# Kernel optimization log

Hardware: AMD Instinct MI355X
Metric: run time of the kernel (lower is better)

The kernel has to match this reference:

```python
import jax, jax.numpy as jnp
import numpy as np

EPS = 1e-5

def _graph_conv(x, src, dst, W, b, N):
    # DGL GraphConv, norm='both': D_out^{-1/2} then aggregate then D_in^{-1/2}
    ones = jnp.ones((src.shape[0],), x.dtype)
    out_deg = jnp.clip(jax.ops.segment_sum(ones, src, num_segments=N), 1.0)
    in_deg = jnp.clip(jax.ops.segment_sum(ones, dst, num_segments=N), 1.0)
    h = (x * (out_deg ** -0.5)[:, None]) @ W          # [N, out] (mult W before gather)
    agg = jax.ops.segment_sum(h[src], dst, num_segments=N)  # [N, out] irregular scatter
    return agg * (in_deg ** -0.5)[:, None] + b

def _bn_relu(h, gamma, beta):
    # BatchNorm1d in training mode: batch stats over node axis (biased var)
    mu = jnp.mean(h, axis=0)
    var = jnp.mean((h - mu) ** 2, axis=0)
    return jax.nn.relu((h - mu) * jax.lax.rsqrt(var + EPS) * gamma + beta)

def setup_inputs() -> dict:
    key = jax.random.key(0)
    ks = jax.random.split(key, 6)
    N, E, F, H, C = 100000, 1000000, 128, 128, 16
    return {
        "x": jax.random.normal(ks[0], (N, F), dtype=jnp.float32),
        "src": jax.random.randint(ks[1], (E,), 0, N, dtype=jnp.int32),
        "dst": jax.random.randint(ks[2], (E,), 0, N, dtype=jnp.int32),
        "W1": jax.random.normal(ks[3], (F, H), dtype=jnp.float32) * 0.05,
        "b1": jnp.zeros((H,), jnp.float32),
        "g1": jnp.ones((H,), jnp.float32),
        "be1": jnp.zeros((H,), jnp.float32),
        "W2": jax.random.normal(ks[4], (H, H), dtype=jnp.float32) * 0.05,
        "b2": jnp.zeros((H,), jnp.float32),
        "g2": jnp.ones((H,), jnp.float32),
        "be2": jnp.zeros((H,), jnp.float32),
        "Wc": jax.random.normal(ks[5], (H, C), dtype=jnp.float32) * 0.05,
        "bc": jnp.zeros((C,), jnp.float32),
    }

def reference(x, src, dst, W1, b1, g1, be1, W2, b2, g2, be2, Wc, bc):
    N = x.shape[0]
    h = _bn_relu(_graph_conv(x, src, dst, W1, b1, N), g1, be1)  # dropout = identity (eval)
    h = _bn_relu(_graph_conv(h, src, dst, W2, b2, N), g2, be2)
    return h @ Wc + bc  # [N, num_cls]
```

## Files before the change

kernel.cpp:

```cpp
#include <hip/hip_runtime.h>

#define FDIM 128
#define MAXDEG 64
#define GATHERB 2048
#define NREP 32

#define RSIZE 128
#define RSHIFT 7
#define RCAP 1024
#define CCAP 14336
#define PCAP 80
#define WCONVB 8

typedef unsigned short ushort_t;
typedef unsigned int uint_t;
typedef __attribute__((ext_vector_type(8))) short short8;
typedef __attribute__((ext_vector_type(16))) float float16;

__device__ __forceinline__ float bflo(uint_t u) { return __uint_as_float(u << 16); }
__device__ __forceinline__ float bfhi(uint_t u) { return __uint_as_float(u & 0xffff0000u); }
__device__ __forceinline__ ushort_t f2bf(float f) {
    uint_t u = __float_as_uint(f);
    return (ushort_t)((u + 0x7fffu + ((u >> 16) & 1u)) >> 16);
}
__device__ __forceinline__ uint_t pack2bf(float lo, float hi) {
    return (uint_t)f2bf(lo) | ((uint_t)f2bf(hi) << 16);
}

__global__ __launch_bounds__(256) void gemm1_kernel(
    const float* __restrict__ x, const ushort_t* __restrict__ wb,
    const int* __restrict__ cs,
    ushort_t* __restrict__ outb, int N) {
    __shared__ ushort_t zt[64][136];
    __shared__ ushort_t wt[128][136];
    __shared__ float csh[64];
    int t = threadIdx.x;
    int base = blockIdx.x * 64;

    const uint4* wb4 = (const uint4*)wb;
    for (int i = t; i < FDIM * 16; i += 256) {
        int n = i >> 4, q = i & 15;
        *(uint4*)&wt[n][q * 8] = wb4[n * 16 + q];
    }
    if (t < 64) {
        int g = base + t;
        csh[t] = (g < N) ? rsqrtf((float)max(cs[g], 1)) : 1.f;
    }
    const float4* x4 = (const float4*)x;
    for (int i = t; i < 64 * 32; i += 256) {
        int row = i >> 5, c4 = i & 31;
        int grow = base + row;
        uint2 o = make_uint2(0u, 0u);
        if (grow < N) {
            float4 v = x4[(size_t)grow * 32 + c4];
            o.x = pack2bf(v.x, v.y);
            o.y = pack2bf(v.z, v.w);
        }
        *(uint2*)&zt[row][c4 * 4] = o;
    }
    __syncthreads();

    int wv = t >> 6, lane = t & 63;
    int rt = wv >> 1;
    int m = lane & 31;
    int kg = lane >> 5;

    short8 af[8];
#pragma unroll
    for (int kk = 0; kk < 8; kk++)
        af[kk] = *(const short8*)&zt[rt * 32 + m][kk * 16 + kg * 8];

#pragma unroll
    for (int cc = 0; cc < 2; cc++) {
        int ct = (wv & 1) * 2 + cc;
        float16 acc = {0, 0, 0, 0, 0, 0, 0, 0, 0, 0, 0, 0, 0, 0, 0, 0};
#pragma unroll
        for (int kk = 0; kk < 8; kk++) {
            short8 bf = *(const short8*)&wt[ct * 32 + m][kk * 16 + kg * 8];
            acc = __builtin_amdgcn_mfma_f32_32x32x16_bf16(af[kk], bf, acc, 0, 0, 0);
        }
        int col = ct * 32 + m;
#pragma unroll
        for (int r = 0; r < 16; r++) {
            int rl = rt * 32 + (r & 3) + 8 * (r >> 2) + 4 * kg;
            int row = base + rl;
            if (row < N) outb[(size_t)row * FDIM + col] = f2bf(acc[r] * csh[rl]);
        }
    }
}

__global__ __launch_bounds__(256) void bucket_kernel(
    const int* __restrict__ src, const int* __restrict__ dst,
    uint_t* __restrict__ bktD, int* __restrict__ baseD,
    uint_t* __restrict__ bktS, int* __restrict__ baseS,
    const float* __restrict__ W1, const float* __restrict__ W2,
    ushort_t* __restrict__ wb1, ushort_t* __restrict__ wb2,
    int E, int P, int R) {
    __shared__ uint4 buf4[CCAP / 4];
    __shared__ int hist[RCAP];
    __shared__ int scanbuf[256];
    uint_t* buf = (uint_t*)buf4;
    int t = threadIdx.x;

    if (blockIdx.x >= 2 * P) {
        int t0 = (blockIdx.x - 2 * P) * 256 + t;
        for (int i = t0; i < FDIM * FDIM; i += WCONVB * 256) {
            int k = i >> 7, n = i & 127;
            wb1[n * FDIM + k] = f2bf(W1[i]);
            wb2[n * FDIM + k] = f2bf(W2[i]);
        }
        return;
    }

    int role = blockIdx.x >= P;
    int p = role ? blockIdx.x - P : blockIdx.x;
    const int* key = role ? src : dst;
    int e0 = p * CCAP;
    int e1 = min(E, e0 + CCAP);
    int cnt = e1 - e0;

    for (int r = t; r < R; r += 256) hist[r] = 0;
    __syncthreads();
    for (int i = e0 + t; i < e1; i += 256) atomicAdd(&hist[key[i] >> RSHIFT], 1);
    __syncthreads();

    int b0 = t * 4;
    int hv[4];
    int s0 = 0;
#pragma unroll
    for (int k = 0; k < 4; k++) {
        hv[k] = (b0 + k < R) ? hist[b0 + k] : 0;
        s0 += hv[k];
    }
    scanbuf[t] = s0;
    __syncthreads();
    for (int off = 1; off < 256; off <<= 1) {
        int v = (t >= off) ? scanbuf[t - off] : 0;
        __syncthreads();
        scanbuf[t] += v;
        __syncthreads();
    }
    int run = scanbuf[t] - s0;
    int* baseG = role ? baseS : baseD;
#pragma unroll
    for (int k = 0; k < 4; k++) {
        if (b0 + k < R) {
            baseG[(b0 + k) * P + p] = run;
            hist[b0 + k] = run;
        }
        run += hv[k];
    }
    if (t == 0) baseG[R * P + p] = cnt;
    __syncthreads();

    for (int i = e0 + t; i < e1; i += 256) {
        int kv = key[i];
        int slot = atomicAdd(&hist[kv >> RSHIFT], 1);
        uint_t entry = role ? (uint_t)kv
                            : (((uint_t)(kv & (RSIZE - 1)) << 25) | (uint_t)src[i]);
        buf[slot] = entry;
    }
    __syncthreads();

    uint_t* outp = role ? bktS : bktD;
    uint4* og = (uint4*)(outp + (size_t)e0);
    int n4 = (cnt + 3) >> 2;
    for (int j = t; j < n4; j += 256) og[j] = buf4[j];
}

__global__ __launch_bounds__(256) void build_kernel(
    const uint_t* __restrict__ bktD, const int* __restrict__ baseD,
    const uint_t* __restrict__ bktS, const int* __restrict__ baseS,
    int* __restrict__ eidx, int* __restrict__ cnt, int* __restrict__ cs,
    int N, int P) {
    __shared__ uint4 ell4[RSIZE][MAXDEG / 4];
    __shared__ int cntN[RSIZE], csN[RSIZE];
    __shared__ int dB0[PCAP], dB1[PCAP], sB0[PCAP], sB1[PCAP];
    uint_t* ell = (uint_t*)ell4;
    int t = threadIdx.x;
    int r = blockIdx.x;

    if (t < RSIZE) { cntN[t] = 0; csN[t] = 0; }
    for (int i = t; i < P; i += 256) {
        dB0[i] = baseD[r * P + i];
        dB1[i] = baseD[(r + 1) * P + i];
        sB0[i] = baseS[r * P + i];
        sB1[i] = baseS[(r + 1) * P + i];
    }
    __syncthreads();

    int wave = t >> 6, lane = t & 63;
    for (int p = wave; p < P; p += 4) {
        int b = dB0[p], len = dB1[p] - b;
        const uint_t* seg = bktD + (size_t)p * CCAP + b;
        for (int i = lane; i < len; i += 64) {
            uint_t e = seg[i];
            int dl = e >> 25;
            uint_t s = e & 0x1FFFFFFu;
            int slot = atomicAdd(&cntN[dl], 1);
            if (slot < MAXDEG) ell[dl * MAXDEG + slot] = s;
        }
        int b2 = sB0[p], len2 = sB1[p] - b2;
        const uint_t* seg2 = bktS + (size_t)p * CCAP + b2;
        for (int i = lane; i < len2; i += 64)
            atomicAdd(&csN[seg2[i] & (RSIZE - 1)], 1);
    }
    __syncthreads();

    int base = r * RSIZE;
    for (int i = t; i < RSIZE * (MAXDEG / 4); i += 256) {
        int n = i >> 4, q = i & 15;
        int g = base + n;
        if (g < N && q * 4 < min(cntN[n], MAXDEG))
            ((uint4*)eidx)[(size_t)g * (MAXDEG / 4) + q] = ell4[n][q];
    }
    if (t < RSIZE) {
        int g = base + t;
        if (g < N) { cnt[g] = cntN[t]; cs[g] = csN[t]; }
    }
}

__global__ __launch_bounds__(256) void gather_kernel(const ushort_t* __restrict__ hb,
                                                     const int* __restrict__ eidx,
                                                     const int* __restrict__ cnt,
                                                     const float* __restrict__ b,
                                                     ushort_t* __restrict__ outb,
                                                     float* __restrict__ statsRep, int N) {
    __shared__ float4 redS[256];
    __shared__ float4 redQ[256];
    int t = threadIdx.x;
    int wave = t >> 6, lane = t & 63;
    int half = lane >> 5, sub = lane & 31;
    const int STRIDE = GATHERB * 4;
    int gw = blockIdx.x * 4 + wave;
    const uint2* h2 = (const uint2*)hb;
    uint2* o2 = (uint2*)outb;
    float4 bb = ((const float4*)b)[sub];
    float st0 = 0, st1 = 0, st2 = 0, st3 = 0, sq0 = 0, sq1 = 0, sq2 = 0, sq3 = 0;

    int node = gw;
    int deg = 0, ridx = 0;
    if (node < N) {
        deg = cnt[node];
        ridx = eidx[(size_t)node * MAXDEG + lane];
    }
    while (node < N) {
        int nnode = node + STRIDE;
        int ndeg = 0, nridx = 0;
        if (nnode < N) {
            ndeg = cnt[nnode];
            nridx = eidx[(size_t)nnode * MAXDEG + lane];
        }

        int e = min(deg, MAXDEG);
        float a0 = 0, a1 = 0, a2 = 0, a3 = 0;
        float c0 = 0, c1 = 0, c2 = 0, c3 = 0;
        int j = 0;
        for (; j + 7 < e; j += 8) {
            int iA = __shfl(ridx, j + half);
            int iB = __shfl(ridx, j + 2 + half);
            int iC = __shfl(ridx, j + 4 + half);
            int iD = __shfl(ridx, j + 6 + half);
            uint2 uA = h2[(size_t)iA * 32 + sub];
            uint2 uB = h2[(size_t)iB * 32 + sub];
            uint2 uC = h2[(size_t)iC * 32 + sub];
            uint2 uD = h2[(size_t)iD * 32 + sub];
            a0 += bflo(uA.x); a1 += bfhi(uA.x); a2 += bflo(uA.y); a3 += bfhi(uA.y);
            c0 += bflo(uB.x); c1 += bfhi(uB.x); c2 += bflo(uB.y); c3 += bfhi(uB.y);
            a0 += bflo(uC.x); a1 += bfhi(uC.x); a2 += bflo(uC.y); a3 += bfhi(uC.y);
            c0 += bflo(uD.x); c1 += bfhi(uD.x); c2 += bflo(uD.y); c3 += bfhi(uD.y);
        }
        for (; j + 3 < e; j += 4) {
            int iA = __shfl(ridx, j + half);
            int iB = __shfl(ridx, j + 2 + half);
            uint2 uA = h2[(size_t)iA * 32 + sub];
            uint2 uB = h2[(size_t)iB * 32 + sub];
            a0 += bflo(uA.x); a1 += bfhi(uA.x); a2 += bflo(uA.y); a3 += bfhi(uA.y);
            c0 += bflo(uB.x); c1 += bfhi(uB.x); c2 += bflo(uB.y); c3 += bfhi(uB.y);
        }
        for (; j < e; j += 2) {
            int jj = j + half;
            bool take = jj < e;
            int i0 = __shfl(ridx, take ? jj : (e - 1));
            float m = take ? 1.f : 0.f;
            uint2 u = h2[(size_t)i0 * 32 + sub];
            a0 = fmaf(bflo(u.x), m, a0); a1 = fmaf(bfhi(u.x), m, a1);
            a2 = fmaf(bflo(u.y), m, a2); a3 = fmaf(bfhi(u.y), m, a3);
        }
        a0 += c0; a1 += c1; a2 += c2; a3 += c3;
        a0 += __shfl_xor(a0, 32);
        a1 += __shfl_xor(a1, 32);
        a2 += __shfl_xor(a2, 32);
        a3 += __shfl_xor(a3, 32);
        if (half == 0) {
            float isc = rsqrtf((float)max(deg, 1));
            uint2 o;
            o.x = pack2bf(fmaf(a0, isc, bb.x), fmaf(a1, isc, bb.y));
            o.y = pack2bf(fmaf(a2, isc, bb.z), fmaf(a3, isc, bb.w));
            o2[(size_t)node * 32 + sub] = o;
            float v0 = bflo(o.x), v1 = bfhi(o.x), v2 = bflo(o.y), v3 = bfhi(o.y);
            st0 += v0; st1 += v1; st2 += v2; st3 += v3;
            sq0 = fmaf(v0, v0, sq0); sq1 = fmaf(v1, v1, sq1);
            sq2 = fmaf(v2, v2, sq2); sq3 = fmaf(v3, v3, sq3);
        }
        node = nnode; deg = ndeg; ridx = nridx;
    }

    redS[t] = make_float4(st0, st1, st2, st3);
    redQ[t] = make_float4(sq0, sq1, sq2, sq3);
    __syncthreads();
    if (t < 32) {
        float4 s = make_float4(0, 0, 0, 0), q = make_float4(0, 0, 0, 0);
#pragma unroll
        for (int w = 0; w < 4; w++) {
            float4 a = redS[w * 64 + t];
            float4 z = redQ[w * 64 + t];
            s.x += a.x; s.y += a.y; s.z += a.z; s.w += a.w;
            q.x += z.x; q.y += z.y; q.z += z.z; q.w += z.w;
        }
        float* dstp = statsRep + (size_t)(blockIdx.x & (NREP - 1)) * 256;
        atomicAdd(&dstp[t * 4 + 0], s.x);
        atomicAdd(&dstp[t * 4 + 1], s.y);
        atomicAdd(&dstp[t * 4 + 2], s.z);
        atomicAdd(&dstp[t * 4 + 3], s.w);
        atomicAdd(&dstp[128 + t * 4 + 0], q.x);
        atomicAdd(&dstp[128 + t * 4 + 1], q.y);
        atomicAdd(&dstp[128 + t * 4 + 2], q.z);
        atomicAdd(&dstp[128 + t * 4 + 3], q.w);
    }
}

__global__ __launch_bounds__(256) void gemm2_kernel(const ushort_t* __restrict__ hb,
                                                    const ushort_t* __restrict__ wb,
                                                    const int* __restrict__ cs,
                                                    const float* __restrict__ statsRep,
                                                    const float* __restrict__ g,
                                                    const float* __restrict__ be,
                                                    ushort_t* __restrict__ outb, int N,
                                                    float invN) {
    __shared__ ushort_t zt[64][136];
    __shared__ ushort_t wt[128][136];
    __shared__ float Ash[FDIM], Bsh[FDIM];
    int t = threadIdx.x;
    int base = blockIdx.x * 64;

    if (t < FDIM) {
        float s = 0.f, q = 0.f;
        for (int r = 0; r < NREP; r++) {
            s += statsRep[r * 256 + t];
            q += statsRep[r * 256 + 128 + t];
        }
        float mu = s * invN;
        float var = q * invN - mu * mu;
        float a = g[t] * rsqrtf(var + 1e-5f);
        Ash[t] = a;
        Bsh[t] = be[t] - mu * a;
    }
    const uint4* wb4 = (const uint4*)wb;
    for (int i = t; i < FDIM * 16; i += 256) {
        int n = i >> 4, q = i & 15;
        *(uint4*)&wt[n][q * 8] = wb4[n * 16 + q];
    }
    __syncthreads();

    const uint_t* h1 = (const uint_t*)hb;
    for (int i = t; i < 64 * 64; i += 256) {
        int row = i >> 6, cp = i & 63;
        int grow = base + row;
        uint_t o = 0;
        if (grow < N) {
            uint_t u = h1[(size_t)grow * 64 + cp];
            float s = rsqrtf((float)max(cs[grow], 1));
            float v0 = fmaxf(fmaf(bflo(u), Ash[cp * 2], Bsh[cp * 2]), 0.f) * s;
            float v1 = fmaxf(fmaf(bfhi(u), Ash[cp * 2 + 1], Bsh[cp * 2 + 1]), 0.f) * s;
            o = pack2bf(v0, v1);
        }
        *(uint_t*)&zt[row][cp * 2] = o;
    }
    __syncthreads();

    int wv = t >> 6, lane = t & 63;
    int rt = wv >> 1;
    int m = lane & 31;
    int kg = lane >> 5;

    short8 af[8];
#pragma unroll
    for (int kk = 0; kk < 8; kk++)
        af[kk] = *(const short8*)&zt[rt * 32 + m][kk * 16 + kg * 8];

#pragma unroll
    for (int cc = 0; cc < 2; cc++) {
        int ct = (wv & 1) * 2 + cc;
        float16 acc = {0, 0, 0, 0, 0, 0, 0, 0, 0, 0, 0, 0, 0, 0, 0, 0};
#pragma unroll
        for (int kk = 0; kk < 8; kk++) {
            short8 bf = *(const short8*)&wt[ct * 32 + m][kk * 16 + kg * 8];
            acc = __builtin_amdgcn_mfma_f32_32x32x16_bf16(af[kk], bf, acc, 0, 0, 0);
        }
        int col = ct * 32 + m;
#pragma unroll
        for (int r = 0; r < 16; r++) {
            int row = base + rt * 32 + (r & 3) + 8 * (r >> 2) + 4 * kg;
            if (row < N) outb[(size_t)row * FDIM + col] = f2bf(acc[r]);
        }
    }
}

__global__ __launch_bounds__(256) void cls_kernel(const ushort_t* __restrict__ hb,
                                                  const float* __restrict__ Wc,
                                                  const float* __restrict__ bc,
                                                  const float* __restrict__ statsRep,
                                                  const float* __restrict__ g,
                                                  const float* __restrict__ be,
                                                  float* __restrict__ out, int N, float invN) {
    __shared__ float wcl[FDIM * 16];
    __shared__ float red[16][256];
    __shared__ float Ash[FDIM], Bsh[FDIM];
    int t = threadIdx.x;
    int base = blockIdx.x * 64;
#pragma unroll
    for (int i = 0; i < 8; i++) wcl[t + i * 256] = Wc[t + i * 256];
    if (t < FDIM) {
        float s = 0.f, q = 0.f;
        for (int r = 0; r < NREP; r++) {
            s += statsRep[r * 256 + t];
            q += statsRep[r * 256 + 128 + t];
        }
        float mu = s * invN;
        float var = q * invN - mu * mu;
        float a = g[t] * rsqrtf(var + 1e-5f);
        Ash[t] = a;
        Bsh[t] = be[t] - mu * a;
    }
    __syncthreads();

    int node = base + (t >> 2);
    int q4 = t & 3;
    float acc[16];
#pragma unroll
    for (int c = 0; c < 16; c++) acc[c] = 0.f;

    if (node < N) {
        const uint2* hu2 = (const uint2*)((const uint_t*)hb + (size_t)node * 64 + q4 * 16);
        const float* Af = Ash + q4 * 32;
        const float* Bf = Bsh + q4 * 32;
#pragma unroll 1
        for (int kk = 0; kk < 8; kk++) {
            uint2 u = hu2[kk];
            float4 ab = *(const float4*)&Af[kk * 4];
            float4 bb = *(const float4*)&Bf[kk * 4];
            float v0 = fmaxf(fmaf(bflo(u.x), ab.x, bb.x), 0.f);
            float v1 = fmaxf(fmaf(bfhi(u.x), ab.y, bb.y), 0.f);
            float v2 = fmaxf(fmaf(bflo(u.y), ab.z, bb.z), 0.f);
            float v3 = fmaxf(fmaf(bfhi(u.y), ab.w, bb.w), 0.f);
            int k0 = q4 * 32 + kk * 4;
            const float* w0 = &wcl[k0 * 16];
#pragma unroll
            for (int c = 0; c < 16; c++) {
                float s = fmaf(v0, w0[c], fmaf(v1, w0[16 + c], fmaf(v2, w0[32 + c], v3 * w0[48 + c])));
                acc[c] += s;
            }
        }
    }
#pragma unroll
    for (int c = 0; c < 16; c++) red[c][t] = acc[c];
    __syncthreads();
#pragma unroll
    for (int i = t; i < 64 * 16; i += 256) {
        int n = i >> 4, c = i & 15;
        float4 p = *(const float4*)&red[c][n * 4];
        int grow = base + n;
        if (grow < N) out[(size_t)grow * 16 + c] = (p.x + p.y) + (p.z + p.w) + bc[c];
    }
}

extern "C" void kernel_launch(void* const* d_in, const int* in_sizes, int n_in,
                              void* d_out, int out_size, void* d_ws, size_t ws_size,
                              hipStream_t stream) {
    const float* x  = (const float*)d_in[0];
    const int* src  = (const int*)d_in[1];
    const int* dst  = (const int*)d_in[2];
    const float* W1 = (const float*)d_in[3];
    const float* b1 = (const float*)d_in[4];
    const float* g1 = (const float*)d_in[5];
    const float* be1= (const float*)d_in[6];
    const float* W2 = (const float*)d_in[7];
    const float* b2 = (const float*)d_in[8];
    const float* g2 = (const float*)d_in[9];
    const float* be2= (const float*)d_in[10];
    const float* Wc = (const float*)d_in[11];
    const float* bc = (const float*)d_in[12];
    float* out = (float*)d_out;

    int N = in_sizes[0] / FDIM;
    int E = in_sizes[1];
    size_t NB = (size_t)N * FDIM;

    ushort_t* bufA = (ushort_t*)d_ws;
    ushort_t* bufB = bufA + NB;
    int* cs        = (int*)(bufB + NB);
    int* cnt       = cs + N;
    float* statsR1 = (float*)(cnt + N);
    float* statsR2 = statsR1 + NREP * 256;
    int* eidx      = (int*)(statsR2 + NREP * 256);
    ushort_t* wb1  = (ushort_t*)(eidx + (size_t)N * MAXDEG);
    ushort_t* wb2  = wb1 + FDIM * FDIM;

    uint_t* bktD = (uint_t*)bufB;
    uint_t* bktS = bktD + (size_t)PCAP * CCAP;
    int* baseD   = (int*)(bktS + (size_t)PCAP * CCAP);
    int* baseS   = baseD + (RCAP + 1) * PCAP;

    int P = (E + CCAP - 1) / CCAP;
    int R = (N + RSIZE - 1) >> RSHIFT;

    hipMemsetAsync(statsR1, 0, (size_t)2 * NREP * 256 * sizeof(float), stream);

    bucket_kernel<<<2 * P + WCONVB, 256, 0, stream>>>(
        src, dst, bktD, baseD, bktS, baseS, W1, W2, wb1, wb2, E, P, R);
    build_kernel<<<R, 256, 0, stream>>>(bktD, baseD, bktS, baseS, eidx, cnt, cs, N, P);

    gemm1_kernel<<<(N + 63) / 64, 256, 0, stream>>>(x, wb1, cs, bufA, N);

    float invN = 1.0f / N;

    gather_kernel<<<GATHERB, 256, 0, stream>>>(bufA, eidx, cnt, b1, bufB, statsR1, N);

    gemm2_kernel<<<(N + 63) / 64, 256, 0, stream>>>(bufB, wb2, cs, statsR1, g1, be1, bufA, N, invN);
    gather_kernel<<<GATHERB, 256, 0, stream>>>(bufA, eidx, cnt, b2, bufB, statsR2, N);

    cls_kernel<<<(N + 63) / 64, 256, 0, stream>>>(bufB, Wc, bc, statsR2, g2, be2, out, N, invN);
}
```

Before: 351.2 us.

## Fuse layer-1 GEMM into bucketing kernel and apply source-degree scaling in gather

The layer-1 GEMM no longer waits for the out-degree counts: it is merged into the bucketing launch as extra blocks that convert W1 to bf16 in shared memory and compute x@W1 without the source normalisation. The out-degree rsqrt scale is applied per edge inside the first gather through a templated path that loads cs for each neighbour and shuffles it across lanes. This removes one kernel launch and the dependency between edge bucketing and the first GEMM, so the two can run concurrently. In exchange the gather does extra per-edge loads and FMAs, each GEMM block redoes the W1 conversion, and CCAP/PCAP are retuned to fit the larger shared-memory footprint.

```diff
diff --git a/kernel.cpp b/kernel.cpp
--- a/kernel.cpp
+++ b/kernel.cpp
@@ -8,8 +8,8 @@
 #define RSIZE 128
 #define RSHIFT 7
 #define RCAP 1024
-#define CCAP 14336
-#define PCAP 80
+#define CCAP 11776
+#define PCAP 96
 #define WCONVB 8
 
 typedef unsigned short ushort_t;
@@ -27,93 +27,90 @@
     return (uint_t)f2bf(lo) | ((uint_t)f2bf(hi) << 16);
 }
 
-__global__ __launch_bounds__(256) void gemm1_kernel(
-    const float* __restrict__ x, const ushort_t* __restrict__ wb,
-    const int* __restrict__ cs,
-    ushort_t* __restrict__ outb, int N) {
-    __shared__ ushort_t zt[64][136];
-    __shared__ ushort_t wt[128][136];
-    __shared__ float csh[64];
-    int t = threadIdx.x;
-    int base = blockIdx.x * 64;
-
-    const uint4* wb4 = (const uint4*)wb;
-    for (int i = t; i < FDIM * 16; i += 256) {
-        int n = i >> 4, q = i & 15;
-        *(uint4*)&wt[n][q * 8] = wb4[n * 16 + q];
-    }
-    if (t < 64) {
-        int g = base + t;
-        csh[t] = (g < N) ? rsqrtf((float)max(cs[g], 1)) : 1.f;
-    }
-    const float4* x4 = (const float4*)x;
-    for (int i = t; i < 64 * 32; i += 256) {
-        int row = i >> 5, c4 = i & 31;
-        int grow = base + row;
-        uint2 o = make_uint2(0u, 0u);
-        if (grow < N) {
-            float4 v = x4[(size_t)grow * 32 + c4];
-            o.x = pack2bf(v.x, v.y);
-            o.y = pack2bf(v.z, v.w);
-        }
-        *(uint2*)&zt[row][c4 * 4] = o;
-    }
-    __syncthreads();
-
-    int wv = t >> 6, lane = t & 63;
-    int rt = wv >> 1;
-    int m = lane & 31;
-    int kg = lane >> 5;
-
-    short8 af[8];
-#pragma unroll
-    for (int kk = 0; kk < 8; kk++)
-        af[kk] = *(const short8*)&zt[rt * 32 + m][kk * 16 + kg * 8];
-
-#pragma unroll
-    for (int cc = 0; cc < 2; cc++) {
-        int ct = (wv & 1) * 2 + cc;
-        float16 acc = {0, 0, 0, 0, 0, 0, 0, 0, 0, 0, 0, 0, 0, 0, 0, 0};
-#pragma unroll
-        for (int kk = 0; kk < 8; kk++) {
-            short8 bf = *(const short8*)&wt[ct * 32 + m][kk * 16 + kg * 8];
-            acc = __builtin_amdgcn_mfma_f32_32x32x16_bf16(af[kk], bf, acc, 0, 0, 0);
-        }
-        int col = ct * 32 + m;
-#pragma unroll
-        for (int r = 0; r < 16; r++) {
-            int rl = rt * 32 + (r & 3) + 8 * (r >> 2) + 4 * kg;
-            int row = base + rl;
-            if (row < N) outb[(size_t)row * FDIM + col] = f2bf(acc[r] * csh[rl]);
-        }
-    }
-}
-
-__global__ __launch_bounds__(256) void bucket_kernel(
+__global__ __launch_bounds__(256) void fused1_kernel(
     const int* __restrict__ src, const int* __restrict__ dst,
     uint_t* __restrict__ bktD, int* __restrict__ baseD,
     uint_t* __restrict__ bktS, int* __restrict__ baseS,
     const float* __restrict__ W1, const float* __restrict__ W2,
-    ushort_t* __restrict__ wb1, ushort_t* __restrict__ wb2,
-    int E, int P, int R) {
-    __shared__ uint4 buf4[CCAP / 4];
-    __shared__ int hist[RCAP];
-    __shared__ int scanbuf[256];
-    uint_t* buf = (uint_t*)buf4;
+    ushort_t* __restrict__ wb2,
+    const float* __restrict__ x, ushort_t* __restrict__ outb,
+    int E, int P, int R, int N, int G1B) {
+    __shared__ __align__(16) char smem[52224];
     int t = threadIdx.x;
-
-    if (blockIdx.x >= 2 * P) {
-        int t0 = (blockIdx.x - 2 * P) * 256 + t;
+    int bid = blockIdx.x;
+
+    if (bid >= 2 * P && bid < 2 * P + WCONVB) {
+        int t0 = (bid - 2 * P) * 256 + t;
         for (int i = t0; i < FDIM * FDIM; i += WCONVB * 256) {
             int k = i >> 7, n = i & 127;
-            wb1[n * FDIM + k] = f2bf(W1[i]);
             wb2[n * FDIM + k] = f2bf(W2[i]);
         }
         return;
     }
 
-    int role = blockIdx.x >= P;
-    int p = role ? blockIdx.x - P : blockIdx.x;
+    if (bid >= 2 * P) {
+        typedef ushort_t row136[136];
+        row136* zt = (row136*)smem;
+        row136* wt = (row136*)(smem + 17408);
+        int idx = bid - 2 * P - WCONVB;
+        if (idx >= G1B) return;
+        int base = idx * 64;
+
+        for (int i = t; i < FDIM * FDIM; i += 256) {
+            int k = i >> 7, n = i & 127;
+            wt[n][k] = f2bf(W1[i]);
+        }
+        const float4* x4 = (const float4*)x;
+        for (int i = t; i < 64 * 32; i += 256) {
+            int row = i >> 5, c4 = i & 31;
+            int grow = base + row;
+            uint2 o = make_uint2(0u, 0u);
+            if (grow < N) {
+                float4 v = x4[(size_t)grow * 32 + c4];
+                o.x = pack2bf(v.x, v.y);
+                o.y = pack2bf(v.z, v.w);
+            }
+            *(uint_t*)&zt[row][c4 * 4] = o.x;
+            *(uint_t*)&zt[row][c4 * 4 + 2] = o.y;
+        }
+        __syncthreads();
+
+        int wv = t >> 6, lane = t & 63;
+        int rt = wv >> 1;
+        int m = lane & 31;
+        int kg = lane >> 5;
+
+        short8 af[8];
+#pragma unroll
+        for (int kk = 0; kk < 8; kk++)
+            af[kk] = *(const short8*)&zt[rt * 32 + m][kk * 16 + kg * 8];
+
+#pragma unroll
+        for (int cc = 0; cc < 2; cc++) {
+            int ct = (wv & 1) * 2 + cc;
+            float16 acc = {0, 0, 0, 0, 0, 0, 0, 0, 0, 0, 0, 0, 0, 0, 0, 0};
+#pragma unroll
+            for (int kk = 0; kk < 8; kk++) {
+                short8 bf = *(const short8*)&wt[ct * 32 + m][kk * 16 + kg * 8];
+                acc = __builtin_amdgcn_mfma_f32_32x32x16_bf16(af[kk], bf, acc, 0, 0, 0);
+            }
+            int col = ct * 32 + m;
+#pragma unroll
+            for (int r = 0; r < 16; r++) {
+                int row = base + rt * 32 + (r & 3) + 8 * (r >> 2) + 4 * kg;
+                if (row < N) outb[(size_t)row * FDIM + col] = f2bf(acc[r]);
+            }
+        }
+        return;
+    }
+
+    uint4* buf4 = (uint4*)smem;
+    int* hist = (int*)(smem + 47104);
+    int* scanbuf = (int*)(smem + 51200);
+    uint_t* buf = (uint_t*)buf4;
+
+    int role = bid >= P;
+    int p = role ? bid - P : bid;
     const int* key = role ? src : dst;
     int e0 = p * CCAP;
     int e1 = min(E, e0 + CCAP);
@@ -220,9 +217,11 @@
     }
 }
 
+template <bool OS>
 __global__ __launch_bounds__(256) void gather_kernel(const ushort_t* __restrict__ hb,
                                                      const int* __restrict__ eidx,
                                                      const int* __restrict__ cnt,
+                                                     const int* __restrict__ cs,
                                                      const float* __restrict__ b,
                                                      ushort_t* __restrict__ outb,
                                                      float* __restrict__ statsRep, int N) {
@@ -240,16 +239,28 @@
 
     int node = gw;
     int deg = 0, ridx = 0;
+    float scv = 0.f;
     if (node < N) {
         deg = cnt[node];
         ridx = eidx[(size_t)node * MAXDEG + lane];
+        if (OS) {
+            int e0 = min(deg, MAXDEG);
+            int s = (lane < e0) ? ridx : 0;
+            scv = rsqrtf((float)max(cs[s], 1));
+        }
     }
     while (node < N) {
         int nnode = node + STRIDE;
         int ndeg = 0, nridx = 0;
+        float nscv = 0.f;
         if (nnode < N) {
             ndeg = cnt[nnode];
             nridx = eidx[(size_t)nnode * MAXDEG + lane];
+            if (OS) {
+                int ne = min(ndeg, MAXDEG);
+                int s = (lane < ne) ? nridx : 0;
+                nscv = rsqrtf((float)max(cs[s], 1));
+            }
         }
 
         int e = min(deg, MAXDEG);
@@ -261,31 +272,43 @@
             int iB = __shfl(ridx, j + 2 + half);
             int iC = __shfl(ridx, j + 4 + half);
             int iD = __shfl(ridx, j + 6 + half);
+            float sA = OS ? __shfl(scv, j + half) : 1.f;
+            float sB = OS ? __shfl(scv, j + 2 + half) : 1.f;
+            float sC = OS ? __shfl(scv, j + 4 + half) : 1.f;
+            float sD = OS ? __shfl(scv, j + 6 + half) : 1.f;
             uint2 uA = h2[(size_t)iA * 32 + sub];
             uint2 uB = h2[(size_t)iB * 32 + sub];
             uint2 uC = h2[(size_t)iC * 32 + sub];
             uint2 uD = h2[(size_t)iD * 32 + sub];
-            a0 += bflo(uA.x); a1 += bfhi(uA.x); a2 += bflo(uA.y); a3 += bfhi(uA.y);
-            c0 += bflo(uB.x); c1 += bfhi(uB.x); c2 += bflo(uB.y); c3 += bfhi(uB.y);
-            a0 += bflo(uC.x); a1 += bfhi(uC.x); a2 += bflo(uC.y); a3 += bfhi(uC.y);
-            c0 += bflo(uD.x); c1 += bfhi(uD.x); c2 += bflo(uD.y); c3 += bfhi(uD.y);
+            a0 = fmaf(bflo(uA.x), sA, a0); a1 = fmaf(bfhi(uA.x), sA, a1);
+            a2 = fmaf(bflo(uA.y), sA, a2); a3 = fmaf(bfhi(uA.y), sA, a3);
+            c0 = fmaf(bflo(uB.x), sB, c0); c1 = fmaf(bfhi(uB.x), sB, c1);
+            c2 = fmaf(bflo(uB.y), sB, c2); c3 = fmaf(bfhi(uB.y), sB, c3);
+            a0 = fmaf(bflo(uC.x), sC, a0); a1 = fmaf(bfhi(uC.x), sC, a1);
+            a2 = fmaf(bflo(uC.y), sC, a2); a3 = fmaf(bfhi(uC.y), sC, a3);
+            c0 = fmaf(bflo(uD.x), sD, c0); c1 = fmaf(bfhi(uD.x), sD, c1);
+            c2 = fmaf(bflo(uD.y), sD, c2); c3 = fmaf(bfhi(uD.y), sD, c3);
         }
         for (; j + 3 < e; j += 4) {
             int iA = __shfl(ridx, j + half);
             int iB = __shfl(ridx, j + 2 + half);
+            float sA = OS ? __shfl(scv, j + half) : 1.f;
+            float sB = OS ? __shfl(scv, j + 2 + half) : 1.f;
             uint2 uA = h2[(size_t)iA * 32 + sub];
             uint2 uB = h2[(size_t)iB * 32 + sub];
-            a0 += bflo(uA.x); a1 += bfhi(uA.x); a2 += bflo(uA.y); a3 += bfhi(uA.y);
-            c0 += bflo(uB.x); c1 += bfhi(uB.x); c2 += bflo(uB.y); c3 += bfhi(uB.y);
+            a0 = fmaf(bflo(uA.x), sA, a0); a1 = fmaf(bfhi(uA.x), sA, a1);
+            a2 = fmaf(bflo(uA.y), sA, a2); a3 = fmaf(bfhi(uA.y), sA, a3);
+            c0 = fmaf(bflo(uB.x), sB, c0); c1 = fmaf(bfhi(uB.x), sB, c1);
+            c2 = fmaf(bflo(uB.y), sB, c2); c3 = fmaf(bfhi(uB.y), sB, c3);
         }
         for (; j < e; j += 2) {
             int jj = j + half;
             bool take = jj < e;
             int i0 = __shfl(ridx, take ? jj : (e - 1));
-            float m = take ? 1.f : 0.f;
+            float s0 = take ? (OS ? __shfl(scv, jj) : 1.f) : 0.f;
             uint2 u = h2[(size_t)i0 * 32 + sub];
-            a0 = fmaf(bflo(u.x), m, a0); a1 = fmaf(bfhi(u.x), m, a1);
-            a2 = fmaf(bflo(u.y), m, a2); a3 = fmaf(bfhi(u.y), m, a3);
+            a0 = fmaf(bflo(u.x), s0, a0); a1 = fmaf(bfhi(u.x), s0, a1);
+            a2 = fmaf(bflo(u.y), s0, a2); a3 = fmaf(bfhi(u.y), s0, a3);
         }
         a0 += c0; a1 += c1; a2 += c2; a3 += c3;
         a0 += __shfl_xor(a0, 32);
@@ -304,6 +327,7 @@
             sq2 = fmaf(v2, v2, sq2); sq3 = fmaf(v3, v3, sq3);
         }
         node = nnode; deg = ndeg; ridx = nridx;
+        if (OS) scv = nscv;
     }
 
     redS[t] = make_float4(st0, st1, st2, st3);
@@ -504,8 +528,7 @@
     float* statsR1 = (float*)(cnt + N);
     float* statsR2 = statsR1 + NREP * 256;
     int* eidx      = (int*)(statsR2 + NREP * 256);
-    ushort_t* wb1  = (ushort_t*)(eidx + (size_t)N * MAXDEG);
-    ushort_t* wb2  = wb1 + FDIM * FDIM;
+    ushort_t* wb2  = (ushort_t*)(eidx + (size_t)N * MAXDEG);
 
     uint_t* bktD = (uint_t*)bufB;
     uint_t* bktS = bktD + (size_t)PCAP * CCAP;
@@ -514,21 +537,20 @@
 
     int P = (E + CCAP - 1) / CCAP;
     int R = (N + RSIZE - 1) >> RSHIFT;
+    int G1B = (N + 63) / 64;
 
     hipMemsetAsync(statsR1, 0, (size_t)2 * NREP * 256 * sizeof(float), stream);
 
-    bucket_kernel<<<2 * P + WCONVB, 256, 0, stream>>>(
-        src, dst, bktD, baseD, bktS, baseS, W1, W2, wb1, wb2, E, P, R);
+    fused1_kernel<<<2 * P + WCONVB + G1B, 256, 0, stream>>>(
+        src, dst, bktD, baseD, bktS, baseS, W1, W2, wb2, x, bufA, E, P, R, N, G1B);
     build_kernel<<<R, 256, 0, stream>>>(bktD, baseD, bktS, baseS, eidx, cnt, cs, N, P);
 
-    gemm1_kernel<<<(N + 63) / 64, 256, 0, stream>>>(x, wb1, cs, bufA, N);
-
     float invN = 1.0f / N;
 
-    gather_kernel<<<GATHERB, 256, 0, stream>>>(bufA, eidx, cnt, b1, bufB, statsR1, N);
+    gather_kernel<true><<<GATHERB, 256, 0, stream>>>(bufA, eidx, cnt, cs, b1, bufB, statsR1, N);
 
     gemm2_kernel<<<(N + 63) / 64, 256, 0, stream>>>(bufB, wb2, cs, statsR1, g1, be1, bufA, N, invN);
-    gather_kernel<<<GATHERB, 256, 0, stream>>>(bufA, eidx, cnt, b2, bufB, statsR2, N);
+    gather_kernel<false><<<GATHERB, 256, 0, stream>>>(bufA, eidx, cnt, nullptr, b2, bufB, statsR2, N);
 
     cls_kernel<<<(N + 63) / 64, 256, 0, stream>>>(bufB, Wc, bc, statsR2, g2, be2, out, N, invN);
 }
```

New measurement: 342.2 us. -2.6%, faster.
